# Kernel optimization log

Measured on AMD Instinct MI355X. Metric: run time of the kernel, lower is better.

Reference implementation:

```python
import jax, jax.numpy as jnp
import numpy as np

DEGREE = 3  # B-spline degree (cubic)


def bspline_basis(x, knots, degree):
    """Cox-de Boor B-spline basis evaluation.
    x: (..., ) values; knots: (K,) non-decreasing knot vector.
    Returns (..., K - degree - 1) basis values.
    """
    xb = x[..., None]
    # degree-0: indicator of half-open knot spans
    B = ((xb >= knots[:-1]) & (xb < knots[1:])).astype(x.dtype)
    # include x == last knot in the final span (standard clamped-spline convention)
    B = B.at[..., -1].set(jnp.where(x == knots[-1], jnp.ones_like(x), B[..., -1]))
    for d in range(1, degree + 1):
        ld = knots[d:-1] - knots[:-(d + 1)]          # left denominators
        rd = knots[d + 1:] - knots[1:-d]             # right denominators
        lterm = jnp.where(ld > 0, (xb - knots[:-(d + 1)]) / jnp.where(ld > 0, ld, 1.0), 0.0) * B[..., :-1]
        rterm = jnp.where(rd > 0, (knots[d + 1:] - xb) / jnp.where(rd > 0, rd, 1.0), 0.0) * B[..., 1:]
        B = lterm + rterm
    return B


def setup_inputs() -> dict:
    key = jax.random.key(0)
    k1, k2, k3 = jax.random.split(key, 3)
    in_feat, out_feat, num_knots, degree = 512, 512, 64, DEGREE
    batch = 2048
    grid_min, grid_max = -1.0, 1.0
    # inputs within grid range so spline bases are active
    x = jax.random.uniform(k1, (batch, in_feat), jnp.float32, grid_min, grid_max)
    # coeffs ~ 0.1 * randn, matching torch init
    coeffs = 0.1 * jax.random.normal(k2, (in_feat, out_feat, num_knots - degree - 1), jnp.float32)
    # xavier-uniform base_weights
    bound = float(np.sqrt(6.0 / (in_feat + out_feat)))
    base_weights = jax.random.uniform(k3, (in_feat, out_feat), jnp.float32, -bound, bound)
    # clamped uniform knot vector: (degree+1) repeats at ends + 56 interior points
    left = jnp.full((degree + 1,), grid_min, jnp.float32)
    right = jnp.full((degree + 1,), grid_max, jnp.float32)
    internal = jnp.linspace(grid_min, grid_max, num_knots - 2 * (degree + 1) + 2, dtype=jnp.float32)[1:-1]
    knots = jnp.concatenate([left, internal, right])
    return {"x": x, "coeffs": coeffs, "base_weights": base_weights, "knots": knots}


def reference(x, coeffs, base_weights, knots):
    # basis: (batch, in_feat, n_basis) -- computed ONCE per input feature
    basis = bspline_basis(x, knots, DEGREE)
    # spline term: sum_j sum_k coeffs[j,o,k] * B_k(x[:,j])
    spline = jnp.einsum('bjk,jok->bo', basis, coeffs)
    # base term: sum_j base_weights[j,o] * SiLU(x[:,j])
    base = jax.nn.silu(x) @ base_weights
    return spline + base
```

## Files before the change

### kernel.cpp

```cpp
#include <hip/hip_runtime.h>
#include <hip/hip_bf16.h>
#include <stdint.h>

#define BATCH 2048
#define INF   512
#define OUTF  512
#define NB    60
#define KP    64
#define LDK   128
#define NJ    64

typedef float    f32x4 __attribute__((ext_vector_type(4)));
typedef unsigned u32x4 __attribute__((ext_vector_type(4)));

__device__ __forceinline__ unsigned short f2bf(float f) {
  unsigned u = __builtin_bit_cast(unsigned, f);
  u += 0x7fff + ((u >> 16) & 1);
  return (unsigned short)(u >> 16);
}

__device__ __forceinline__ void gll16(const void* g, void* l) {
  __builtin_amdgcn_global_load_lds(
      (const __attribute__((address_space(1))) void*)g,
      (__attribute__((address_space(3))) void*)l, 16, 0, 0);
}

__global__ __launch_bounds__(256) void prep_ct(const float* __restrict__ coeffs,
                                               const float* __restrict__ bw,
                                               unsigned short* __restrict__ CT) {
  int tg  = blockIdx.x * 256 + threadIdx.x;
  int row = tg >> 3;
  int pos = tg & 7;
  const float* src = coeffs + (long)row * NB;
  unsigned short v[8];
  if (pos < 7) {
    float4 c0 = *(const float4*)(src + pos * 8);
    float4 c1 = *(const float4*)(src + pos * 8 + 4);
    v[0]=f2bf(c0.x); v[1]=f2bf(c0.y); v[2]=f2bf(c0.z); v[3]=f2bf(c0.w);
    v[4]=f2bf(c1.x); v[5]=f2bf(c1.y); v[6]=f2bf(c1.z); v[7]=f2bf(c1.w);
  } else {
    float4 c0 = *(const float4*)(src + 56);
    v[0]=f2bf(c0.x); v[1]=f2bf(c0.y); v[2]=f2bf(c0.z); v[3]=f2bf(c0.w);
    v[4]=f2bf(bw[row]); v[5]=0; v[6]=0; v[7]=0;
  }
  uint4 pack;
  pack.x = (unsigned)v[0] | ((unsigned)v[1] << 16);
  pack.y = (unsigned)v[2] | ((unsigned)v[3] << 16);
  pack.z = (unsigned)v[4] | ((unsigned)v[5] << 16);
  pack.w = (unsigned)v[6] | ((unsigned)v[7] << 16);
  *(uint4*)(CT + (long)row * KP + pos * 8) = pack;
}

__global__ __launch_bounds__(256) void basis_kernel(const float* __restrict__ x,
                                                    const float* __restrict__ knots,
                                                    uint4* __restrict__ recs) {
  __shared__ float xl[64][65];
  __shared__ float Uk[64];
  int t  = threadIdx.x;
  int bt = blockIdx.x & 31, jt = blockIdx.x >> 5;
  int b0 = bt * 64, j0 = jt * 64;
  if (t < 64) Uk[t] = knots[t];
  for (int it = 0; it < 16; ++it) {
    int f = it * 256 + t;
    int r = f >> 6, c = f & 63;
    xl[r][c] = x[(long)(b0 + r) * INF + j0 + c];
  }
  __syncthreads();
  int bl = t & 63;
  int jg = t >> 6;
  for (int jj = 0; jj < 16; ++jj) {
    int jl = jg * 16 + jj;
    float xv = xl[bl][jl];
    int i = (int)floorf((xv + 1.0f) * 28.5f);
    i = max(0, min(56, i));
    if (xv < Uk[i + 3]) i--;
    else if (xv >= Uk[i + 4]) i++;
    i = max(0, min(56, i));
    int m = i + 3;
    float l1 = xv - Uk[m],     r1 = Uk[m + 1] - xv;
    float l2 = xv - Uk[m - 1], r2 = Uk[m + 2] - xv;
    float l3 = xv - Uk[m - 2], r3 = Uk[m + 3] - xv;
    float N0 = 1.0f, N1, N2, N3, temp, saved;
    temp = N0 / (r1 + l1); N0 = r1 * temp; N1 = l1 * temp;
    temp = N0 / (r1 + l2); N0 = r1 * temp; saved = l2 * temp;
    temp = N1 / (r2 + l1); N1 = saved + r2 * temp; N2 = l1 * temp;
    temp = N0 / (r1 + l3); N0 = r1 * temp; saved = l3 * temp;
    temp = N1 / (r2 + l2); N1 = saved + r2 * temp; saved = l2 * temp;
    temp = N2 / (r3 + l1); N2 = saved + r3 * temp; N3 = l1 * temp;
    float sil = xv / (1.0f + __expf(-xv));
    uint4 rec;
    rec.x = (unsigned)f2bf(N0) | ((unsigned)f2bf(N1) << 16);
    rec.y = (unsigned)f2bf(N2) | ((unsigned)f2bf(N3) << 16);
    rec.z = (unsigned)f2bf(sil) | ((unsigned)i << 16);
    rec.w = 0;
    recs[(long)(j0 + jl) * BATCH + b0 + bl] = rec;
  }
}

__global__ __launch_bounds__(256, 2) void gemm_kernel(const unsigned short* __restrict__ CT,
                                                      const uint4* __restrict__ recs,
                                                      float* __restrict__ out) {
  __shared__ __align__(16) unsigned short Bl[2][128 * KP];
  __shared__ __align__(16) unsigned short Al[2][128 * KP];
  int t = threadIdx.x;
  int lane = t & 63, wid = t >> 6;
  int bx = blockIdx.x;
  int kt = bx & 7, mt = (bx >> 3) & 15, nt = bx >> 7;
  int b0 = mt * 128, o0 = nt * 128, j0 = kt * 64;
  int wr = wid >> 1, wc = wid & 1;
  int r  = t & 127;
  int eh = t >> 7;

  f32x4 acc[4][4];
#pragma unroll
  for (int mm = 0; mm < 4; ++mm)
#pragma unroll
    for (int nn = 0; nn < 4; ++nn) { f32x4 z = {0.f, 0.f, 0.f, 0.f}; acc[mm][nn] = z; }

#pragma unroll
  for (int it = 0; it < 8; ++it)
    ((uint4*)Al)[it * 256 + t] = make_uint4(0, 0, 0, 0);

#pragma unroll
  for (int it = 0; it < 4; ++it) {
    int g = it * 256 + t, o = g >> 3, ls = g & 7, ks = ls ^ (o & 7);
    gll16(CT + ((long)(j0 * 512 + o0 + o) << 6) + ks * 8,
          (char*)Bl + (it * 256 + wid * 64) * 16);
  }
  uint4 recA = recs[(long)j0 * BATCH + b0 + r];
  uint4 recB;
  int olds0 = 0, olds1 = 0;
  asm volatile("s_waitcnt lgkmcnt(0)" ::: "memory");

#define CLR(K)                                                                   \
  if ((K) < s || (K) > s + 3)                                                    \
    *(unsigned short*)(A + r * LDK + ((((K) >> 3) ^ (r & 7)) << 4) + ((K) & 7) * 2) = 0;
#define PUT(K, V)                                                                \
  *(unsigned short*)(A + r * LDK + ((((K) >> 3) ^ (r & 7)) << 4) + ((K) & 7) * 2) = (unsigned short)(V);

#define BODY(CUR, JJ, RECUSE, RECLOAD, OLDS)                                     \
  {                                                                              \
    if ((JJ) + 1 < NJ) {                                                         \
      int jn = j0 + (JJ) + 1;                                                    \
      _Pragma("unroll")                                                          \
      for (int it = 0; it < 4; ++it) {                                           \
        int g = it * 256 + t, o = g >> 3, ls = g & 7, ks = ls ^ (o & 7);         \
        gll16(CT + ((long)(jn * 512 + o0 + o) << 6) + ks * 8,                    \
              (char*)Bl + (1 - (CUR)) * 16384 + (it * 256 + wid * 64) * 16);     \
      }                                                                          \
      RECLOAD = recs[(long)jn * BATCH + b0 + r];                                 \
      asm volatile("s_waitcnt vmcnt(5)" ::: "memory");                           \
    } else {                                                                     \
      asm volatile("s_waitcnt vmcnt(0)" ::: "memory");                           \
    }                                                                            \
    __builtin_amdgcn_s_barrier();            \
    {                                                                            \
      char* A = (char*)Al + (CUR) * 16384;                                       \
      int s = (int)(RECUSE.z >> 16);                                             \
      if (eh == 0) {                                                             \
        int k0 = OLDS, k1 = OLDS + 1;                                            \
        CLR(k0) CLR(k1)                                                          \
        PUT(s,     RECUSE.x)                                                     \
        PUT(s + 1, RECUSE.x >> 16)                                               \
      } else {                                                                   \
        int k0 = OLDS + 2, k1 = OLDS + 3;                                        \
        CLR(k0) CLR(k1)                                                          \
        PUT(s + 2, RECUSE.y)                                                     \
        PUT(s + 3, RECUSE.y >> 16)                                               \
        *(unsigned short*)(A + r * LDK + ((7 ^ (r & 7)) << 4) + 8) = (unsigned short)RECUSE.z; \
      }                                                                          \
      OLDS = s;                                                                  \
    }                                                                            \
    asm volatile("s_waitcnt lgkmcnt(0)" ::: "memory");                           \
    __builtin_amdgcn_s_barrier();                           \
    {                                                                            \
      const char* A = (const char*)Al + (CUR) * 16384;                           \
      const char* B = (const char*)Bl + (CUR) * 16384;                           \
      _Pragma("unroll")                                                          \
      for (int kp = 0; kp < 2; ++kp) {                                           \
        int ksl = kp * 4 + (lane >> 4);                                          \
        u32x4 av[4], bv[4];                                                      \
        _Pragma("unroll")                                                        \
        for (int mm = 0; mm < 4; ++mm) {                                         \
          int row = wr * 64 + mm * 16 + (lane & 15);                             \
          av[mm] = *(const u32x4*)(A + row * LDK + ((ksl ^ (row & 7)) << 4));    \
        }                                                                        \
        _Pragma("unroll")                                                        \
        for (int nn = 0; nn < 4; ++nn) {                                         \
          int col = wc * 64 + nn * 16 + (lane & 15);                             \
          bv[nn] = *(const u32x4*)(B + col * LDK + ((ksl ^ (col & 7)) << 4));    \
        }                                                                        \
        _Pragma("unroll")                                                        \
        for (int mm = 0; mm < 4; ++mm)                                           \
          _Pragma("unroll")                                                      \
          for (int nn = 0; nn < 4; ++nn)                                         \
            asm volatile("v_mfma_f32_16x16x32_bf16 %0, %1, %2, %0"               \
                         : "+v"(acc[mm][nn]) : "v"(av[mm]), "v"(bv[nn]));        \
      }                                                                          \
    }                                                                            \
    asm volatile("s_waitcnt lgkmcnt(0)" ::: "memory");                           \
    __builtin_amdgcn_s_barrier();            \
  }

  for (int jt = 0; jt < 32; ++jt) {
    BODY(0, 2 * jt,     recA, recB, olds0)
    BODY(1, 2 * jt + 1, recB, recA, olds1)
  }
#undef BODY
#undef CLR
#undef PUT

  int r0 = (lane >> 4) * 4, c0 = lane & 15;
#pragma unroll
  for (int mm = 0; mm < 4; ++mm)
#pragma unroll
    for (int nn = 0; nn < 4; ++nn) {
      int grow = b0 + wr * 64 + mm * 16 + r0;
      int gcol = o0 + wc * 64 + nn * 16 + c0;
#pragma unroll
      for (int e = 0; e < 4; ++e)
        unsafeAtomicAdd(&out[(long)(grow + e) * OUTF + gcol], acc[mm][nn][e]);
    }
}

extern "C" void kernel_launch(void* const* d_in, const int* in_sizes, int n_in,
                              void* d_out, int out_size, void* d_ws, size_t ws_size,
                              hipStream_t stream) {
  const float* x      = (const float*)d_in[0];
  const float* coeffs = (const float*)d_in[1];
  const float* bw     = (const float*)d_in[2];
  const float* knots  = (const float*)d_in[3];
  float* out = (float*)d_out;

  const size_t CT_BYTES  = (size_t)INF * OUTF * KP * 2;
  const size_t REC_BYTES = (size_t)INF * BATCH * 16;
  if (ws_size < CT_BYTES + REC_BYTES) return;

  unsigned short* CT = (unsigned short*)d_ws;
  uint4* recs = (uint4*)((char*)d_ws + CT_BYTES);

  hipMemsetAsync(d_out, 0, (size_t)BATCH * OUTF * sizeof(float), stream);
  prep_ct<<<(INF * OUTF * 8) / 256, 256, 0, stream>>>(coeffs, bw, CT);
  basis_kernel<<<(BATCH / 64) * (INF / 64), 256, 0, stream>>>(x, knots, recs);
  gemm_kernel<<<512, 256, 0, stream>>>(CT, recs, out);
}
```

Before: 114.3 us.

## Fuse prep kernels and software-pipeline sparse A-tile scatter one step ahead

Merges the coefficient-conversion and basis-record kernels into one launch that splits work by block index, which saves a kernel launch and lets the two phases overlap. In the GEMM main loop, the sparse A-tile entries for the next step are written into the alternate LDS buffer while the current step's MFMAs run, and record loads are issued two steps ahead. This removes one barrier and one wait per iteration. It adds a prologue, a peeled tail and more delicate vmcnt accounting, which carries correctness risk.

```diff
diff --git a/kernel.cpp b/kernel.cpp
--- a/kernel.cpp
+++ b/kernel.cpp
@@ -25,39 +25,41 @@
       (__attribute__((address_space(3))) void*)l, 16, 0, 0);
 }
 
-__global__ __launch_bounds__(256) void prep_ct(const float* __restrict__ coeffs,
-                                               const float* __restrict__ bw,
-                                               unsigned short* __restrict__ CT) {
-  int tg  = blockIdx.x * 256 + threadIdx.x;
-  int row = tg >> 3;
-  int pos = tg & 7;
-  const float* src = coeffs + (long)row * NB;
-  unsigned short v[8];
-  if (pos < 7) {
-    float4 c0 = *(const float4*)(src + pos * 8);
-    float4 c1 = *(const float4*)(src + pos * 8 + 4);
-    v[0]=f2bf(c0.x); v[1]=f2bf(c0.y); v[2]=f2bf(c0.z); v[3]=f2bf(c0.w);
-    v[4]=f2bf(c1.x); v[5]=f2bf(c1.y); v[6]=f2bf(c1.z); v[7]=f2bf(c1.w);
-  } else {
-    float4 c0 = *(const float4*)(src + 56);
-    v[0]=f2bf(c0.x); v[1]=f2bf(c0.y); v[2]=f2bf(c0.z); v[3]=f2bf(c0.w);
-    v[4]=f2bf(bw[row]); v[5]=0; v[6]=0; v[7]=0;
-  }
-  uint4 pack;
-  pack.x = (unsigned)v[0] | ((unsigned)v[1] << 16);
-  pack.y = (unsigned)v[2] | ((unsigned)v[3] << 16);
-  pack.z = (unsigned)v[4] | ((unsigned)v[5] << 16);
-  pack.w = (unsigned)v[6] | ((unsigned)v[7] << 16);
-  *(uint4*)(CT + (long)row * KP + pos * 8) = pack;
-}
-
-__global__ __launch_bounds__(256) void basis_kernel(const float* __restrict__ x,
-                                                    const float* __restrict__ knots,
-                                                    uint4* __restrict__ recs) {
+__global__ __launch_bounds__(256) void prep_fused(const float* __restrict__ coeffs,
+                                                  const float* __restrict__ bw,
+                                                  const float* __restrict__ x,
+                                                  const float* __restrict__ knots,
+                                                  unsigned short* __restrict__ CT,
+                                                  uint4* __restrict__ recs) {
   __shared__ float xl[64][65];
   __shared__ float Uk[64];
+  if (blockIdx.x < 8192) {
+    int tg  = blockIdx.x * 256 + threadIdx.x;
+    int row = tg >> 3;
+    int pos = tg & 7;
+    const float* src = coeffs + (long)row * NB;
+    unsigned short v[8];
+    if (pos < 7) {
+      float4 c0 = *(const float4*)(src + pos * 8);
+      float4 c1 = *(const float4*)(src + pos * 8 + 4);
+      v[0]=f2bf(c0.x); v[1]=f2bf(c0.y); v[2]=f2bf(c0.z); v[3]=f2bf(c0.w);
+      v[4]=f2bf(c1.x); v[5]=f2bf(c1.y); v[6]=f2bf(c1.z); v[7]=f2bf(c1.w);
+    } else {
+      float4 c0 = *(const float4*)(src + 56);
+      v[0]=f2bf(c0.x); v[1]=f2bf(c0.y); v[2]=f2bf(c0.z); v[3]=f2bf(c0.w);
+      v[4]=f2bf(bw[row]); v[5]=0; v[6]=0; v[7]=0;
+    }
+    uint4 pack;
+    pack.x = (unsigned)v[0] | ((unsigned)v[1] << 16);
+    pack.y = (unsigned)v[2] | ((unsigned)v[3] << 16);
+    pack.z = (unsigned)v[4] | ((unsigned)v[5] << 16);
+    pack.w = (unsigned)v[6] | ((unsigned)v[7] << 16);
+    *(uint4*)(CT + (long)row * KP + pos * 8) = pack;
+    return;
+  }
+  int bid = blockIdx.x - 8192;
   int t  = threadIdx.x;
-  int bt = blockIdx.x & 31, jt = blockIdx.x >> 5;
+  int bt = bid & 31, jt = bid >> 5;
   int b0 = bt * 64, j0 = jt * 64;
   if (t < 64) Uk[t] = knots[t];
   for (int it = 0; it < 16; ++it) {
@@ -120,6 +122,7 @@
 #pragma unroll
   for (int it = 0; it < 8; ++it)
     ((uint4*)Al)[it * 256 + t] = make_uint4(0, 0, 0, 0);
+  __syncthreads();
 
 #pragma unroll
   for (int it = 0; it < 4; ++it) {
@@ -127,10 +130,27 @@
     gll16(CT + ((long)(j0 * 512 + o0 + o) << 6) + ks * 8,
           (char*)Bl + (it * 256 + wid * 64) * 16);
   }
-  uint4 recA = recs[(long)j0 * BATCH + b0 + r];
-  uint4 recB;
-  int olds0 = 0, olds1 = 0;
-  asm volatile("s_waitcnt lgkmcnt(0)" ::: "memory");
+  uint4 rec0 = recs[(long)j0 * BATCH + b0 + r];
+  uint4 recB = recs[(long)(j0 + 1) * BATCH + b0 + r];
+  uint4 recA;
+  int olds0, olds1 = 0;
+  {
+    char* A = (char*)Al;
+    int s = (int)(rec0.z >> 16);
+    if (eh == 0) {
+      *(unsigned short*)(A + r * LDK + (((s >> 3) ^ (r & 7)) << 4) + (s & 7) * 2) = (unsigned short)rec0.x;
+      int k = s + 1;
+      *(unsigned short*)(A + r * LDK + (((k >> 3) ^ (r & 7)) << 4) + (k & 7) * 2) = (unsigned short)(rec0.x >> 16);
+    } else {
+      int k2 = s + 2, k3 = s + 3;
+      *(unsigned short*)(A + r * LDK + (((k2 >> 3) ^ (r & 7)) << 4) + (k2 & 7) * 2) = (unsigned short)rec0.y;
+      *(unsigned short*)(A + r * LDK + (((k3 >> 3) ^ (r & 7)) << 4) + (k3 & 7) * 2) = (unsigned short)(rec0.y >> 16);
+      *(unsigned short*)(A + r * LDK + ((7 ^ (r & 7)) << 4) + 8) = (unsigned short)rec0.z;
+    }
+    olds0 = s;
+  }
+  asm volatile("s_waitcnt vmcnt(1) lgkmcnt(0)" ::: "memory");
+  __builtin_amdgcn_s_barrier();
 
 #define CLR(K)                                                                   \
   if ((K) < s || (K) > s + 3)                                                    \
@@ -138,7 +158,7 @@
 #define PUT(K, V)                                                                \
   *(unsigned short*)(A + r * LDK + ((((K) >> 3) ^ (r & 7)) << 4) + ((K) & 7) * 2) = (unsigned short)(V);
 
-#define BODY(CUR, JJ, RECUSE, RECLOAD, OLDS)                                     \
+#define BODY(CUR, JJ, RECUSE, RECLOAD, OLDSNXT, VMSTR)                           \
   {                                                                              \
     if ((JJ) + 1 < NJ) {                                                         \
       int jn = j0 + (JJ) + 1;                                                    \
@@ -148,31 +168,26 @@
         gll16(CT + ((long)(jn * 512 + o0 + o) << 6) + ks * 8,                    \
               (char*)Bl + (1 - (CUR)) * 16384 + (it * 256 + wid * 64) * 16);     \
       }                                                                          \
-      RECLOAD = recs[(long)jn * BATCH + b0 + r];                                 \
-      asm volatile("s_waitcnt vmcnt(5)" ::: "memory");                           \
-    } else {                                                                     \
-      asm volatile("s_waitcnt vmcnt(0)" ::: "memory");                           \
     }                                                                            \
-    __builtin_amdgcn_s_barrier();            \
-    {                                                                            \
-      char* A = (char*)Al + (CUR) * 16384;                                       \
+    if ((JJ) + 2 < NJ)                                                           \
+      RECLOAD = recs[(long)(j0 + (JJ) + 2) * BATCH + b0 + r];                    \
+    if ((JJ) + 1 < NJ) {                                                         \
+      char* A = (char*)Al + (1 - (CUR)) * 16384;                                 \
       int s = (int)(RECUSE.z >> 16);                                             \
       if (eh == 0) {                                                             \
-        int k0 = OLDS, k1 = OLDS + 1;                                            \
+        int k0 = OLDSNXT, k1 = OLDSNXT + 1;                                      \
         CLR(k0) CLR(k1)                                                          \
         PUT(s,     RECUSE.x)                                                     \
         PUT(s + 1, RECUSE.x >> 16)                                               \
       } else {                                                                   \
-        int k0 = OLDS + 2, k1 = OLDS + 3;                                        \
+        int k0 = OLDSNXT + 2, k1 = OLDSNXT + 3;                                  \
         CLR(k0) CLR(k1)                                                          \
         PUT(s + 2, RECUSE.y)                                                     \
         PUT(s + 3, RECUSE.y >> 16)                                               \
         *(unsigned short*)(A + r * LDK + ((7 ^ (r & 7)) << 4) + 8) = (unsigned short)RECUSE.z; \
       }                                                                          \
-      OLDS = s;                                                                  \
+      OLDSNXT = s;                                                               \
     }                                                                            \
-    asm volatile("s_waitcnt lgkmcnt(0)" ::: "memory");                           \
-    __builtin_amdgcn_s_barrier();                           \
     {                                                                            \
       const char* A = (const char*)Al + (CUR) * 16384;                           \
       const char* B = (const char*)Bl + (CUR) * 16384;                           \
@@ -198,14 +213,16 @@
                          : "+v"(acc[mm][nn]) : "v"(av[mm]), "v"(bv[nn]));        \
       }                                                                          \
     }                                                                            \
-    asm volatile("s_waitcnt lgkmcnt(0)" ::: "memory");                           \
-    __builtin_amdgcn_s_barrier();            \
-  }
-
-  for (int jt = 0; jt < 32; ++jt) {
-    BODY(0, 2 * jt,     recA, recB, olds0)
-    BODY(1, 2 * jt + 1, recB, recA, olds1)
-  }
+    asm volatile("s_waitcnt " VMSTR " lgkmcnt(0)" ::: "memory");                 \
+    __builtin_amdgcn_s_barrier();                                                \
+  }
+
+  for (int jt = 0; jt < 31; ++jt) {
+    BODY(0, 2 * jt,     recB, recA, olds1, "vmcnt(1)")
+    BODY(1, 2 * jt + 1, recA, recB, olds0, "vmcnt(1)")
+  }
+  BODY(0, 62, recB, recA, olds1, "vmcnt(0)")
+  BODY(1, 63, recA, recB, olds0, "vmcnt(0)")
 #undef BODY
 #undef CLR
 #undef PUT
@@ -240,7 +257,6 @@
   uint4* recs = (uint4*)((char*)d_ws + CT_BYTES);
 
   hipMemsetAsync(d_out, 0, (size_t)BATCH * OUTF * sizeof(float), stream);
-  prep_ct<<<(INF * OUTF * 8) / 256, 256, 0, stream>>>(coeffs, bw, CT);
-  basis_kernel<<<(BATCH / 64) * (INF / 64), 256, 0, stream>>>(x, knots, recs);
+  prep_fused<<<8192 + 256, 256, 0, stream>>>(coeffs, bw, x, knots, CT, recs);
   gemm_kernel<<<512, 256, 0, stream>>>(CT, recs, out);
 }
```

Result: slower. 133.1 us (+16.5%).
